# Kernel optimization log

Measured on AMD Instinct MI355X. Metric: run time of the kernel, lower is better.

Reference implementation:

```python
import jax, jax.numpy as jnp
import numpy as np

EMBED = 768
HEADS = 12
FACTOR = 2
LN_EPS = 1e-5


def layer_norm(x, gamma, beta):
    mu = jnp.mean(x, axis=-1, keepdims=True)
    var = jnp.mean(jnp.square(x - mu), axis=-1, keepdims=True)
    return (x - mu) * jax.lax.rsqrt(var + LN_EPS) * gamma + beta


def setup_inputs() -> dict:
    key = jax.random.key(0)
    ks = jax.random.split(key, 8)
    B, S, E = 8, 1024, EMBED
    H = FACTOR * E
    s_e = 1.0 / np.sqrt(E)
    s_h = 1.0 / np.sqrt(H)
    return {
        "x": jax.random.normal(ks[0], (B, S, E), jnp.float32),
        "Wq": jax.random.normal(ks[1], (E, E), jnp.float32) * s_e,
        "Wk": jax.random.normal(ks[2], (E, E), jnp.float32) * s_e,
        "Wv": jax.random.normal(ks[3], (E, E), jnp.float32) * s_e,
        "W1": jax.random.normal(ks[4], (E, H), jnp.float32) * s_e,
        "b1": jnp.zeros((H,), jnp.float32),
        "W2": jax.random.normal(ks[5], (H, E), jnp.float32) * s_h,
        "b2": jnp.zeros((E,), jnp.float32),
        "g1": jnp.ones((E,), jnp.float32),
        "beta1": jnp.zeros((E,), jnp.float32),
        "g2": jnp.ones((E,), jnp.float32),
        "beta2": jnp.zeros((E,), jnp.float32),
    }


def reference(x, Wq, Wk, Wv, W1, b1, W2, b2, g1, beta1, g2, beta2):
    B, S, E = x.shape
    hd = E // HEADS
    # NOTE: original reshapes (B,S,E)->(B,H,S,hd) WITHOUT transposing heads
    # (non-standard: mixes sequence blocks across heads) - replicated faithfully.
    q = (x @ Wq).reshape(B, HEADS, S, hd)
    k = (x @ Wk).reshape(B, HEADS, S, hd)
    v = (x @ Wv).reshape(B, HEADS, S, hd)
    # no 1/sqrt(d) scaling in the original
    attn = jax.nn.softmax(jnp.einsum('bnqd,bnkd->bnqk', q, k), axis=-1)
    # NOTE: original einsum 'bnqk,bnvd->bnqd' sums over BOTH k and v
    # (value is sum-pooled over its sequence axis) - replicated faithfully.
    out = jnp.einsum('bnqk,bnvd->bnqd', attn, v)
    out = out.transpose(0, 2, 1, 3).reshape(B, S, E)
    a = x + layer_norm(out, g1, beta1)
    # GELU after BOTH linears (exact GELU, torch default)
    h = jax.nn.gelu(a @ W1 + b1, approximate=False)
    m = jax.nn.gelu(h @ W2 + b2, approximate=False)
    return x + layer_norm(m, g2, beta2)
```

## Files before the change

kernel.cpp:

```cpp
#include <hip/hip_runtime.h>
#include <hip/hip_bf16.h>
#include <math.h>

#define E_ 768
#define HID_ 1536
#define SQ_ 1024

typedef unsigned short u16;
using bf16x8 = __attribute__((ext_vector_type(8))) __bf16;
using f32x4  = __attribute__((ext_vector_type(4))) float;

__device__ __forceinline__ u16 f2bf(float f) {
  union { float f; unsigned u; } v; v.f = f;
  unsigned r = v.u + 0x7FFFu + ((v.u >> 16) & 1u);
  return (u16)(r >> 16);
}
__device__ __forceinline__ float bf2f(u16 h) {
  union { unsigned u; float f; } v; v.u = ((unsigned)h) << 16; return v.f;
}
__device__ __forceinline__ float gelu_f(float x) {
  return 0.5f * x * (1.0f + erff(x * 0.70710678118654752f));
}

#define GLDS16(gp, sp) __builtin_amdgcn_global_load_lds( \
    (__attribute__((address_space(1))) const void*)(const void*)(gp), \
    (__attribute__((address_space(3))) void*)(void*)(sp), 16, 0, 0)

__global__ void prep_kernel(const float* __restrict__ x, const float* __restrict__ W1,
                            const float* __restrict__ W2, u16* __restrict__ xb,
                            u16* __restrict__ W1T, u16* __restrict__ W2T,
                            float* __restrict__ Rp, float* __restrict__ Y) {
  __shared__ float T[64 * 65];
  int bid = blockIdx.x, t = threadIdx.x;
  if (bid >= 6720) {
    int rb = bid - 6720;
    int r = rb >> 2, c = rb & 3;
    int b = r / 12, n = r % 12;
    if (rb == 0) {
#pragma unroll
      for (int i = 0; i < 24; ++i) Y[t + i * 256] = 0.f;
    }
    int u0 = n << 10;
    int s_lo = u0 / 12;
    int s_hi = (u0 + 1023) / 12;
    int cnt = s_hi - s_lo + 1;
    int cs = s_lo + (cnt * c) / 4;
    int ce = s_lo + (cnt * (c + 1)) / 4;
    float acc[12][3];
#pragma unroll
    for (int g = 0; g < 12; ++g)
      for (int q = 0; q < 3; ++q) acc[g][q] = 0.f;
    const float* xp = x + (size_t)b * SQ_ * E_;
    for (int s = cs; s < ce; ++s) {
      float v0 = xp[(size_t)s * E_ + t];
      float v1 = xp[(size_t)s * E_ + t + 256];
      float v2 = xp[(size_t)s * E_ + t + 512];
      int du = 12 * s - u0;
#pragma unroll
      for (int g = 0; g < 12; ++g) {
        int u = du + g;
        if (u >= 0 && u < 1024) { acc[g][0] += v0; acc[g][1] += v1; acc[g][2] += v2; }
      }
    }
    float* Rr = Rp + (size_t)rb * 9216;
#pragma unroll
    for (int g = 0; g < 12; ++g) {
      Rr[g * 768 + t]       = acc[g][0];
      Rr[g * 768 + t + 256] = acc[g][1];
      Rr[g * 768 + t + 512] = acc[g][2];
    }
    return;
  }
  if (bid < 6144) {
    int base = bid * 1024 + t * 4;
    const float4 v = *reinterpret_cast<const float4*>(x + base);
    ushort4 o; o.x = f2bf(v.x); o.y = f2bf(v.y); o.z = f2bf(v.z); o.w = f2bf(v.w);
    *reinterpret_cast<ushort4*>(xb + base) = o;
    return;
  }
  const float* in; u16* out; int R_in, C_in, rt, ct;
  if (bid < 6432) {
    int b2 = bid - 6144; in = W1; out = W1T; R_in = 768; C_in = 1536;
    rt = b2 / 24; ct = b2 % 24;
  } else {
    int b3 = bid - 6432; in = W2; out = W2T; R_in = 1536; C_in = 768;
    rt = b3 / 12; ct = b3 % 12;
  }
  int r0 = rt << 6, c0 = ct << 6;
  int tr = t >> 4, tc4 = (t & 15) << 2;
#pragma unroll
  for (int i = 0; i < 4; ++i) {
    int row = tr + (i << 4);
    const float4 v = *reinterpret_cast<const float4*>(in + (size_t)(r0 + row) * C_in + c0 + tc4);
    T[row * 65 + tc4 + 0] = v.x;
    T[row * 65 + tc4 + 1] = v.y;
    T[row * 65 + tc4 + 2] = v.z;
    T[row * 65 + tc4 + 3] = v.w;
  }
  __syncthreads();
#pragma unroll
  for (int i = 0; i < 4; ++i) {
    int orow = tr + (i << 4);
    ushort4 o;
    o.x = f2bf(T[(tc4 + 0) * 65 + orow]);
    o.y = f2bf(T[(tc4 + 1) * 65 + orow]);
    o.z = f2bf(T[(tc4 + 2) * 65 + orow]);
    o.w = f2bf(T[(tc4 + 3) * 65 + orow]);
    *reinterpret_cast<ushort4*>(out + (size_t)(c0 + orow) * R_in + r0 + tc4) = o;
  }
}

__global__ __launch_bounds__(256, 4) void yfin_kernel(
    const float* __restrict__ Rp, const float* __restrict__ Wv,
    float* __restrict__ Y) {
  int bid = blockIdx.x;
  int r = bid >> 2, jq = bid & 3;
  int t = threadIdx.x;
  __shared__ float Ls[12 * 192];
  __shared__ float red[4][12][64];
  const float* Rb = Rp + (size_t)r * 4 * 9216 + jq * 192;
  for (int i = t; i < 576; i += 256) {
    int g = i / 48, off = (i % 48) << 2;
    const float* p = Rb + g * 768 + off;
    float4 v0 = *reinterpret_cast<const float4*>(p);
    float4 v1 = *reinterpret_cast<const float4*>(p + 9216);
    float4 v2 = *reinterpret_cast<const float4*>(p + 18432);
    float4 v3 = *reinterpret_cast<const float4*>(p + 27648);
    float4 s4;
    s4.x = (v0.x + v1.x) + (v2.x + v3.x);
    s4.y = (v0.y + v1.y) + (v2.y + v3.y);
    s4.z = (v0.z + v1.z) + (v2.z + v3.z);
    s4.w = (v0.w + v1.w) + (v2.w + v3.w);
    *reinterpret_cast<float4*>(&Ls[g * 192 + off]) = s4;
  }
  __syncthreads();
  int d = t & 63, sub = t >> 6;
  float part[12];
#pragma unroll
  for (int g = 0; g < 12; ++g) part[g] = 0.f;
  int jl0 = sub * 48;
  const float* wp = Wv + (size_t)(jq * 192) * 768 + d;
  for (int jj = 0; jj < 48; ++jj) {
    int jl = jl0 + jj;
    const float* wj = wp + (size_t)jl * 768;
#pragma unroll
    for (int g = 0; g < 12; ++g)
      part[g] += Ls[g * 192 + jl] * wj[g * 64];
  }
#pragma unroll
  for (int g = 0; g < 12; ++g) red[sub][g][d] = part[g];
  __syncthreads();
  if (t < 64) {
    float s = 0.f;
#pragma unroll
    for (int su = 0; su < 4; ++su)
#pragma unroll
      for (int g = 0; g < 12; ++g) s += red[su][g][t];
    atomicAdd(&Y[r * 64 + t], s);
  }
}

__global__ void c1_kernel(const float* __restrict__ Y, const float* __restrict__ g1,
                          const float* __restrict__ be1, const float* __restrict__ W1,
                          const float* __restrict__ b1, float* __restrict__ C1) {
  int bid = blockIdx.x;
  int b = bid / 48, c = bid % 48;
  int t = threadIdx.x;
  __shared__ float Ls[768];
  __shared__ float red[8][32];
  __shared__ float red2[8];
  float y0 = Y[b * 768 + t];
  float y1 = Y[b * 768 + t + 256];
  float y2 = Y[b * 768 + t + 512];
  float s = y0 + y1 + y2;
  float sq = y0 * y0 + y1 * y1 + y2 * y2;
#pragma unroll
  for (int o = 32; o > 0; o >>= 1) { s += __shfl_down(s, o, 64); sq += __shfl_down(sq, o, 64); }
  if ((t & 63) == 0) { red2[(t >> 6) * 2] = s; red2[(t >> 6) * 2 + 1] = sq; }
  __syncthreads();
  s  = red2[0] + red2[2] + red2[4] + red2[6];
  sq = red2[1] + red2[3] + red2[5] + red2[7];
  float mu = s * (1.f / 768.f);
  float var = sq * (1.f / 768.f) - mu * mu;
  float rsv = rsqrtf(var + 1e-5f);
  Ls[t]       = (y0 - mu) * rsv * g1[t]       + be1[t];
  Ls[t + 256] = (y1 - mu) * rsv * g1[t + 256] + be1[t + 256];
  Ls[t + 512] = (y2 - mu) * rsv * g1[t + 512] + be1[t + 512];
  __syncthreads();
  int tc = t & 31, ts = t >> 5;
  int n = c * 32 + tc;
  float acc = 0.f;
  int j0 = ts * 96;
#pragma unroll 4
  for (int j = j0; j < j0 + 96; ++j) acc += Ls[j] * W1[(size_t)j * HID_ + n];
  red[ts][tc] = acc;
  __syncthreads();
  if (ts == 0) {
    float sv = b1[n];
#pragma unroll
    for (int k = 0; k < 8; ++k) sv += red[k][tc];
    C1[b * HID_ + n] = sv;
  }
}

template <int MODE>
__global__ __launch_bounds__(256, 2) void gemm_bt_kernel(
    const u16* __restrict__ A, const u16* __restrict__ BT,
    const float* __restrict__ bias, void* __restrict__ out0, void* __restrict__ out1,
    int N, int lda, int ldb) {
  __shared__ __align__(16) u16 As[128 * 64];
  __shared__ __align__(16) u16 Bs[128 * 64];
  int bid = blockIdx.x;
  int xcd = bid & 7, idx = bid >> 3;
  int mloc, n_, k_off, kk = 0;
  if (MODE == 0) { mloc = idx / 12; n_ = idx % 12; k_off = 0; }
  else           { kk = idx / 48; int rem = idx % 48; mloc = rem / 6; n_ = rem % 6; k_off = kk * 768; }
  int bm = (xcd * 8 + mloc) << 7, bn = n_ << 7;

  int t = threadIdx.x;
  int lane = t & 63, w = t >> 6;
  int wm = (w >> 1) << 6, wn = (w & 1) << 6;
  int quad = lane >> 4, l16 = lane & 15;
  f32x4 acc[4][4] = {};

  for (int k0 = 0; k0 < 768; k0 += 64) {
    __syncthreads();
#pragma unroll
    for (int i = 0; i < 4; ++i) {
      int ci = t + (i << 8);
      int r = ci >> 3, csw = ci & 7;
      int kc = csw ^ (r & 7);
      const u16* ga = A + (size_t)(bm + r) * lda + k_off + k0 + (kc << 3);
      GLDS16(ga, As + ci * 8);
      const u16* gb = BT + (size_t)(bn + r) * ldb + k_off + k0 + (kc << 3);
      GLDS16(gb, Bs + ci * 8);
    }
    __builtin_amdgcn_s_waitcnt(0);
    __syncthreads();
#pragma unroll
    for (int ks = 0; ks < 2; ++ks) {
      bf16x8 af[4], bf[4];
      int kc = (ks << 2) + quad;
#pragma unroll
      for (int mt = 0; mt < 4; ++mt) {
        int row = wm + (mt << 4) + l16;
        af[mt] = *reinterpret_cast<const bf16x8*>(As + row * 64 + ((kc ^ (row & 7)) << 3));
      }
#pragma unroll
      for (int nt = 0; nt < 4; ++nt) {
        int row = wn + (nt << 4) + l16;
        bf[nt] = *reinterpret_cast<const bf16x8*>(Bs + row * 64 + ((kc ^ (row & 7)) << 3));
      }
#pragma unroll
      for (int mt = 0; mt < 4; ++mt)
#pragma unroll
        for (int nt = 0; nt < 4; ++nt)
          acc[mt][nt] = __builtin_amdgcn_mfma_f32_16x16x32_bf16(af[mt], bf[nt], acc[mt][nt], 0, 0, 0);
    }
  }

#pragma unroll
  for (int mt = 0; mt < 4; ++mt) {
    int row0 = bm + wm + (mt << 4) + (quad << 2);
#pragma unroll
    for (int nt = 0; nt < 4; ++nt) {
      int col = bn + wn + (nt << 4) + l16;
      float bv = (MODE == 0) ? bias[(bm >> 10) * N + col] : 0.f;
#pragma unroll
      for (int rr = 0; rr < 4; ++rr) {
        float v = acc[mt][nt][rr] + bv;
        size_t idxo = (size_t)(row0 + rr) * N + col;
        if (MODE == 0)       ((u16*)out0)[idxo] = f2bf(gelu_f(v));
        else if (kk == 0)    ((u16*)out0)[idxo] = f2bf(v);
        else                 ((u16*)out1)[idxo] = f2bf(v);
      }
    }
  }
}

__global__ void ln2_kernel(const u16* __restrict__ p0, const u16* __restrict__ p1,
                           const float* __restrict__ x, const float* __restrict__ b2,
                           const float* __restrict__ g2, const float* __restrict__ be2,
                           float* __restrict__ out) {
  int row = blockIdx.x, t = threadIdx.x;
  int e = t << 2;
  ushort4 pa = *reinterpret_cast<const ushort4*>(p0 + (size_t)row * 768 + e);
  ushort4 pb = *reinterpret_cast<const ushort4*>(p1 + (size_t)row * 768 + e);
  float4 bb = *reinterpret_cast<const float4*>(b2 + e);
  float v0 = gelu_f(bf2f(pa.x) + bf2f(pb.x) + bb.x);
  float v1 = gelu_f(bf2f(pa.y) + bf2f(pb.y) + bb.y);
  float v2 = gelu_f(bf2f(pa.z) + bf2f(pb.z) + bb.z);
  float v3 = gelu_f(bf2f(pa.w) + bf2f(pb.w) + bb.w);
  float s = (v0 + v1) + (v2 + v3);
  float sq = (v0 * v0 + v1 * v1) + (v2 * v2 + v3 * v3);
  __shared__ float red[8];
#pragma unroll
  for (int o = 32; o > 0; o >>= 1) { s += __shfl_down(s, o, 64); sq += __shfl_down(sq, o, 64); }
  if ((t & 63) == 0) { red[(t >> 6) * 2] = s; red[(t >> 6) * 2 + 1] = sq; }
  __syncthreads();
  s  = red[0] + red[2] + red[4];
  sq = red[1] + red[3] + red[5];
  float mu = s * (1.f / 768.f);
  float var = sq * (1.f / 768.f) - mu * mu;
  float rs = rsqrtf(var + 1e-5f);
  float4 gg = *reinterpret_cast<const float4*>(g2 + e);
  float4 be = *reinterpret_cast<const float4*>(be2 + e);
  float4 xx = *reinterpret_cast<const float4*>(x + (size_t)row * 768 + e);
  float4 o;
  o.x = xx.x + (v0 - mu) * rs * gg.x + be.x;
  o.y = xx.y + (v1 - mu) * rs * gg.y + be.y;
  o.z = xx.z + (v2 - mu) * rs * gg.z + be.z;
  o.w = xx.w + (v3 - mu) * rs * gg.w + be.w;
  *reinterpret_cast<float4*>(out + (size_t)row * 768 + e) = o;
}

extern "C" void kernel_launch(void* const* d_in, const int* in_sizes, int n_in,
                              void* d_out, int out_size, void* d_ws, size_t ws_size,
                              hipStream_t stream) {
  const float* x   = (const float*)d_in[0];
  const float* Wv  = (const float*)d_in[3];
  const float* W1  = (const float*)d_in[4];
  const float* b1  = (const float*)d_in[5];
  const float* W2  = (const float*)d_in[6];
  const float* b2  = (const float*)d_in[7];
  const float* g1  = (const float*)d_in[8];
  const float* be1 = (const float*)d_in[9];
  const float* g2  = (const float*)d_in[10];
  const float* be2 = (const float*)d_in[11];
  float* out = (float*)d_out;

  char* ws = (char*)d_ws;
  u16*   xb  = (u16*)(ws);
  u16*   W1T = (u16*)(ws + 12582912);
  u16*   W2T = (u16*)(ws + 14942208);
  u16*   h   = (u16*)(ws + 17301504);
  float* Rp  = (float*)(ws + 17301504);
  float* Y   = (float*)(ws + 44826624);
  float* C1  = (float*)(ws + 44875776);
  u16*   m0  = (u16*)(ws + 44924928);
  u16*   p1  = xb;

  prep_kernel<<<7104, 256, 0, stream>>>(x, W1, W2, xb, W1T, W2T, Rp, Y);
  yfin_kernel<<<384, 256, 0, stream>>>(Rp, Wv, Y);
  c1_kernel<<<384, 256, 0, stream>>>(Y, g1, be1, W1, b1, C1);
  gemm_bt_kernel<0><<<768, 256, 0, stream>>>(xb, W1T, C1, (void*)h, nullptr, 1536, 768, 768);
  gemm_bt_kernel<1><<<768, 256, 0, stream>>>(h, W2T, nullptr, (void*)m0, (void*)p1, 768, 1536, 1536);
  ln2_kernel<<<8192, 192, 0, stream>>>(m0, p1, x, b2, g2, be2, out);
}
```

Before: 215.0 us.

## Rewrite GEMM as 256x256 tiles with double-buffered LDS ping-pong pipeline

The bf16 GEMM kernel now uses 256x256 output tiles with 512 threads (8 waves, each 128x64) instead of 128x128 with 256 threads. LDS is double-buffered, and global-to-LDS staging of the next K chunk is interleaved with quarter-tile MFMA phases. Barriers and setprio raise MFMA priority over loads. The aim is to hide global load latency and raise arithmetic intensity. In exchange the grid drops to 192 blocks, which underfills the GPU's CUs, and it adds many barriers and much more LDS (128KB) per block.

```diff
diff --git a/kernel.cpp b/kernel.cpp
--- a/kernel.cpp
+++ b/kernel.cpp
@@ -204,63 +204,136 @@
 }
 
 template <int MODE>
-__global__ __launch_bounds__(256, 2) void gemm_bt_kernel(
+__global__ __launch_bounds__(512, 2) void gemm_bt_kernel(
     const u16* __restrict__ A, const u16* __restrict__ BT,
     const float* __restrict__ bias, void* __restrict__ out0, void* __restrict__ out1,
     int N, int lda, int ldb) {
-  __shared__ __align__(16) u16 As[128 * 64];
-  __shared__ __align__(16) u16 Bs[128 * 64];
+  __shared__ __align__(16) u16 As0[256 * 64], As1[256 * 64];
+  __shared__ __align__(16) u16 Bs0[256 * 64], Bs1[256 * 64];
   int bid = blockIdx.x;
   int xcd = bid & 7, idx = bid >> 3;
-  int mloc, n_, k_off, kk = 0;
-  if (MODE == 0) { mloc = idx / 12; n_ = idx % 12; k_off = 0; }
-  else           { kk = idx / 48; int rem = idx % 48; mloc = rem / 6; n_ = rem % 6; k_off = kk * 768; }
-  int bm = (xcd * 8 + mloc) << 7, bn = n_ << 7;
+  int mtile, ntile, k_off, kk = 0;
+  if (MODE == 0) { mtile = xcd * 4 + idx / 6; ntile = idx % 6; k_off = 0; }
+  else           { kk = idx / 12; int rem = idx % 12; mtile = xcd * 4 + rem / 3; ntile = rem % 3; k_off = kk * 768; }
+  int bm = mtile << 8, bn = ntile << 8;
 
   int t = threadIdx.x;
   int lane = t & 63, w = t >> 6;
-  int wm = (w >> 1) << 6, wn = (w & 1) << 6;
+  int wm = (w >> 2) << 7, wn = (w & 3) << 6;
   int quad = lane >> 4, l16 = lane & 15;
-  f32x4 acc[4][4] = {};
-
-  for (int k0 = 0; k0 < 768; k0 += 64) {
-    __syncthreads();
-#pragma unroll
-    for (int i = 0; i < 4; ++i) {
-      int ci = t + (i << 8);
-      int r = ci >> 3, csw = ci & 7;
-      int kc = csw ^ (r & 7);
-      const u16* ga = A + (size_t)(bm + r) * lda + k_off + k0 + (kc << 3);
-      GLDS16(ga, As + ci * 8);
-      const u16* gb = BT + (size_t)(bn + r) * ldb + k_off + k0 + (kc << 3);
-      GLDS16(gb, Bs + ci * 8);
-    }
-    __builtin_amdgcn_s_waitcnt(0);
-    __syncthreads();
-#pragma unroll
-    for (int ks = 0; ks < 2; ++ks) {
-      bf16x8 af[4], bf[4];
-      int kc = (ks << 2) + quad;
-#pragma unroll
-      for (int mt = 0; mt < 4; ++mt) {
-        int row = wm + (mt << 4) + l16;
-        af[mt] = *reinterpret_cast<const bf16x8*>(As + row * 64 + ((kc ^ (row & 7)) << 3));
+  f32x4 acc[8][4] = {};
+  bf16x8 af[4][2], bf[4][2];
+
+  int ci0 = t, ci1 = t + 512;
+  int sr0 = ci0 >> 3, sr1 = ci1 >> 3;
+  size_t aof0 = (size_t)sr0 * lda + ((((ci0 & 7) ^ (sr0 & 7))) << 3);
+  size_t aof1 = (size_t)sr1 * lda + ((((ci1 & 7) ^ (sr1 & 7))) << 3);
+  size_t bof0 = (size_t)sr0 * ldb + ((((ci0 & 7) ^ (sr0 & 7))) << 3);
+  size_t bof1 = (size_t)sr1 * ldb + ((((ci1 & 7) ^ (sr1 & 7))) << 3);
+  int ldso0 = ci0 << 3, ldso1 = ci1 << 3;
+
+  const u16* Ab = A + (size_t)bm * lda + k_off;
+  const u16* Ab2 = Ab + (size_t)128 * lda;
+  const u16* Bb = BT + (size_t)bn * ldb + k_off;
+  const u16* Bb2 = Bb + (size_t)128 * ldb;
+
+  auto STG_A = [&](u16* dst, const u16* src) {
+    GLDS16(src + aof0, dst + ldso0);
+    GLDS16(src + aof1, dst + ldso1);
+  };
+  auto STG_B = [&](u16* dst, const u16* src) {
+    GLDS16(src + bof0, dst + ldso0);
+    GLDS16(src + bof1, dst + ldso1);
+  };
+  auto LDA = [&](const u16* as, int m0t) {
+#pragma unroll
+    for (int mt = 0; mt < 4; ++mt)
+#pragma unroll
+      for (int ks = 0; ks < 2; ++ks) {
+        int row = wm + ((m0t + mt) << 4) + l16;
+        int kc = (ks << 2) + quad;
+        af[mt][ks] = *reinterpret_cast<const bf16x8*>(as + row * 64 + ((kc ^ (row & 7)) << 3));
       }
-#pragma unroll
-      for (int nt = 0; nt < 4; ++nt) {
-        int row = wn + (nt << 4) + l16;
-        bf[nt] = *reinterpret_cast<const bf16x8*>(Bs + row * 64 + ((kc ^ (row & 7)) << 3));
+  };
+  auto LDB = [&](const u16* bs, int n0t) {
+#pragma unroll
+    for (int nt = 0; nt < 2; ++nt)
+#pragma unroll
+      for (int ks = 0; ks < 2; ++ks) {
+        int row = wn + ((n0t + nt) << 4) + l16;
+        int kc = (ks << 2) + quad;
+        bf[n0t + nt][ks] = *reinterpret_cast<const bf16x8*>(bs + row * 64 + ((kc ^ (row & 7)) << 3));
       }
-#pragma unroll
-      for (int mt = 0; mt < 4; ++mt)
-#pragma unroll
-        for (int nt = 0; nt < 4; ++nt)
-          acc[mt][nt] = __builtin_amdgcn_mfma_f32_16x16x32_bf16(af[mt], bf[nt], acc[mt][nt], 0, 0, 0);
-    }
-  }
-
-#pragma unroll
-  for (int mt = 0; mt < 4; ++mt) {
+  };
+  auto MM = [&](int ma, int na) {
+    __builtin_amdgcn_s_setprio(1);
+#pragma unroll
+    for (int mt = 0; mt < 4; ++mt)
+#pragma unroll
+      for (int nt = 0; nt < 2; ++nt)
+#pragma unroll
+        for (int ks = 0; ks < 2; ++ks)
+          acc[ma + mt][na + nt] =
+              __builtin_amdgcn_mfma_f32_16x16x32_bf16(af[mt][ks], bf[na + nt][ks], acc[ma + mt][na + nt], 0, 0, 0);
+    __builtin_amdgcn_s_setprio(0);
+  };
+
+  STG_A(As0, Ab);          STG_A(As0 + 8192, Ab2);
+  STG_B(Bs0, Bb);          STG_B(Bs0 + 8192, Bb2);
+  STG_A(As1, Ab + 64);
+  asm volatile("s_waitcnt vmcnt(2)" ::: "memory");
+  __builtin_amdgcn_s_barrier();
+
+  for (int it = 0; it < 6; ++it) {
+    int c1o = (2 * it + 1) << 6;
+    int c2o = (2 * it + 2) << 6;
+    int c3o = (2 * it + 3) << 6;
+    bool st = (it < 5);
+    LDA(As0, 0); LDB(Bs0, 0);
+    STG_A(As1 + 8192, Ab2 + c1o);
+    __builtin_amdgcn_s_barrier();
+    MM(0, 0);
+    __builtin_amdgcn_s_barrier();
+    LDB(Bs0, 2);
+    STG_B(Bs1, Bb + c1o);
+    __builtin_amdgcn_s_barrier();
+    MM(0, 2);
+    __builtin_amdgcn_s_barrier();
+    LDA(As0, 4);
+    STG_B(Bs1 + 8192, Bb2 + c1o);
+    __builtin_amdgcn_s_barrier();
+    MM(4, 2);
+    __builtin_amdgcn_s_barrier();
+    if (st) STG_A(As0, Ab + c2o);
+    __builtin_amdgcn_s_barrier();
+    MM(4, 0);
+    if (st) asm volatile("s_waitcnt vmcnt(2)" ::: "memory");
+    else    asm volatile("s_waitcnt vmcnt(0)" ::: "memory");
+    __builtin_amdgcn_s_barrier();
+    LDA(As1, 0); LDB(Bs1, 0);
+    if (st) STG_A(As0 + 8192, Ab2 + c2o);
+    __builtin_amdgcn_s_barrier();
+    MM(0, 0);
+    __builtin_amdgcn_s_barrier();
+    LDB(Bs1, 2);
+    if (st) STG_B(Bs0, Bb + c2o);
+    __builtin_amdgcn_s_barrier();
+    MM(0, 2);
+    __builtin_amdgcn_s_barrier();
+    LDA(As1, 4);
+    if (st) STG_B(Bs0 + 8192, Bb2 + c2o);
+    __builtin_amdgcn_s_barrier();
+    MM(4, 2);
+    __builtin_amdgcn_s_barrier();
+    if (st) STG_A(As1, Ab + c3o);
+    __builtin_amdgcn_s_barrier();
+    MM(4, 0);
+    if (st) asm volatile("s_waitcnt vmcnt(2)" ::: "memory");
+    __builtin_amdgcn_s_barrier();
+  }
+
+#pragma unroll
+  for (int mt = 0; mt < 8; ++mt) {
     int row0 = bm + wm + (mt << 4) + (quad << 2);
 #pragma unroll
     for (int nt = 0; nt < 4; ++nt) {
@@ -343,7 +416,7 @@
   prep_kernel<<<7104, 256, 0, stream>>>(x, W1, W2, xb, W1T, W2T, Rp, Y);
   yfin_kernel<<<384, 256, 0, stream>>>(Rp, Wv, Y);
   c1_kernel<<<384, 256, 0, stream>>>(Y, g1, be1, W1, b1, C1);
-  gemm_bt_kernel<0><<<768, 256, 0, stream>>>(xb, W1T, C1, (void*)h, nullptr, 1536, 768, 768);
-  gemm_bt_kernel<1><<<768, 256, 0, stream>>>(h, W2T, nullptr, (void*)m0, (void*)p1, 768, 1536, 1536);
+  gemm_bt_kernel<0><<<192, 512, 0, stream>>>(xb, W1T, C1, (void*)h, nullptr, 1536, 768, 768);
+  gemm_bt_kernel<1><<<192, 512, 0, stream>>>(h, W2T, nullptr, (void*)m0, (void*)p1, 768, 1536, 1536);
   ln2_kernel<<<8192, 192, 0, stream>>>(m0, p1, x, b2, g2, be2, out);
 }
```

Result: slower. 232.4 us (+8.0%).
